# Performance work log

Measured on AMD Instinct MI355X. Metric: run time of the kernel, lower is better.

The kernel has to match this reference:

```python
import jax, jax.numpy as jnp
import numpy as np

B, S, C = 2, 2048, 1024
U, H = 1024, 16
FFH = int(U * 4.0)
NEG = -1e9
EPS = 1e-5


def setup_inputs() -> dict:
    key = jax.random.key(0)
    ks = jax.random.split(key, 16)
    w = lambda k, sh: jax.random.normal(k, sh, dtype=jnp.float32) * 0.02
    return {
        'x': jax.random.normal(ks[0], (B, S, C), dtype=jnp.float32),
        'wq': w(ks[1], (C, U)), 'bq': jnp.zeros((U,), jnp.float32),
        'wk': w(ks[2], (C, U)), 'bk': jnp.zeros((U,), jnp.float32),
        'wv': w(ks[3], (C, U)), 'bv': jnp.zeros((U,), jnp.float32),
        'wf1': w(ks[4], (U, FFH)), 'bf1': jnp.zeros((FFH,), jnp.float32),
        'wf2': w(ks[5], (FFH, U)), 'bf2': jnp.zeros((U,), jnp.float32),
        'ln_g': jnp.ones((S, U), jnp.float32), 'ln_b': jnp.zeros((S, U), jnp.float32),
        'ffln_g': jnp.ones((S, U), jnp.float32), 'ffln_b': jnp.zeros((S, U), jnp.float32),
    }


def _ln2d(x, g, b):
    # LayerNorm over last two dims ([len_ts, units]) as in nn.LayerNorm([S, U])
    m = jnp.mean(x, axis=(-2, -1), keepdims=True)
    v = jnp.mean(jnp.square(x - m), axis=(-2, -1), keepdims=True)
    return (x - m) * jax.lax.rsqrt(v + EPS) * g + b


def reference(x, wq, bq, wk, bk, wv, bv, wf1, bf1, wf2, bf2, ln_g, ln_b, ffln_g, ffln_b):
    dh = U // H
    Q = (x @ wq + bq).reshape(B, S, H, dh)
    K = (x @ wk + bk).reshape(B, S, H, dh)
    V = (x @ wv + bv).reshape(B, S, H, dh)
    scores = jnp.einsum('bqhd,bkhd->bhqk', Q, K) / jnp.sqrt(jnp.float32(dh))
    mask = jnp.tril(jnp.ones((S, S), dtype=bool))  # causal tril buffer
    scores = jnp.where(mask, scores, NEG)
    attn = jax.nn.softmax(scores, axis=-1)
    out = jnp.einsum('bhqk,bkhd->bqhd', attn, V).reshape(B, S, U)
    out = out + x  # residual
    out = _ln2d(out, ln_g, ln_b)
    ff = jax.nn.relu(out @ wf1 + bf1) @ wf2 + bf2
    out = _ln2d(out + ff, ffln_g, ffln_b)
    return out
```

## Files before the change

kernel.cpp:

```cpp
#include <hip/hip_runtime.h>
#include <hip/hip_bf16.h>

typedef short s16x8 __attribute__((ext_vector_type(8)));
typedef float f32x4 __attribute__((ext_vector_type(4)));
typedef float f32x16 __attribute__((ext_vector_type(16)));
typedef unsigned short u16x4 __attribute__((ext_vector_type(4)));
typedef unsigned u32x4 __attribute__((ext_vector_type(4)));

#define DEV static __device__ __forceinline__

DEV unsigned short f2bf(float f) {
  __hip_bfloat16 h = __float2bfloat16(f);
  return *reinterpret_cast<unsigned short*>(&h);
}
DEV float bf2f(unsigned short u) {
  union { unsigned u; float f; } v; v.u = (unsigned)u << 16; return v.f;
}

#define GLDS16(src, dst) \
  __builtin_amdgcn_global_load_lds((const __attribute__((address_space(1))) void*)(src), \
                                   (__attribute__((address_space(3))) void*)(dst), 16, 0, 0)

#define MFMA(a, b, c) __builtin_amdgcn_mfma_f32_16x16x32_bf16((a), (b), (c), 0, 0, 0)
#define MFMA32(a, b, c) __builtin_amdgcn_mfma_f32_32x32x16_bf16((a), (b), (c), 0, 0, 0)

__global__ __launch_bounds__(256) void k_f32_to_bf16(const float* __restrict__ in,
                                                     unsigned short* __restrict__ out, int n4) {
  int i = blockIdx.x * 256 + threadIdx.x;
  if (i >= n4) return;
  float4 v = ((const float4*)in)[i];
  u16x4 o; o.x = f2bf(v.x); o.y = f2bf(v.y); o.z = f2bf(v.z); o.w = f2bf(v.w);
  ((u16x4*)out)[i] = o;
}

__global__ __launch_bounds__(256) void k_transpose_w(const float* __restrict__ W,
                                                     unsigned short* __restrict__ Wt,
                                                     int K, int N, float scale) {
  __shared__ float t[64][65];
  int k0 = blockIdx.x * 64, n0 = blockIdx.y * 64;
  int tid = threadIdx.x;
#pragma unroll
  for (int i = 0; i < 16; ++i) {
    int idx = tid + i * 256; int r = idx >> 6, c = idx & 63;
    t[r][c] = W[(size_t)(k0 + r) * N + (n0 + c)];
  }
  __syncthreads();
#pragma unroll
  for (int i = 0; i < 16; ++i) {
    int idx = tid + i * 256; int r = idx >> 6, c = idx & 63;
    Wt[(size_t)(n0 + r) * K + (k0 + c)] = f2bf(t[c][r] * scale);
  }
}

__global__ void k_concat3(const float* __restrict__ a, const float* __restrict__ b,
                          const float* __restrict__ c, float* __restrict__ out, int n, float sa) {
  int i = blockIdx.x * 256 + threadIdx.x;
  if (i >= 3 * n) return;
  int j = (i < n) ? i : (i < 2 * n ? i - n : i - 2 * n);
  out[i] = (i < n) ? a[j] * sa : (i < 2 * n ? b[j] : c[j]);
}

template <int MODE>
__global__ __launch_bounds__(512, 2) void k_gemm8(
    const unsigned short* __restrict__ A, int lda,
    const unsigned short* __restrict__ Bt, int ldb,
    const float* __restrict__ bias,
    unsigned short* __restrict__ Cb, float* __restrict__ Cf, int ldc,
    int K, int nnt, size_t zstride,
    unsigned short* __restrict__ Cq, unsigned short* __restrict__ Ck,
    unsigned short* __restrict__ Cv) {
  __shared__ __align__(16) unsigned short As[2 * 2 * 8192];
  __shared__ __align__(16) unsigned short Bs[2 * 2 * 8192];
  int nwg = gridDim.x;
  int bid = blockIdx.x;
  int cpx = nwg >> 3;
  int swz = (bid & 7) * cpx + (bid >> 3);
  int mt = swz / nnt, nt = swz % nnt;
  int m0 = mt * 256, n0 = nt * 256;
  int tid = threadIdx.x, w = tid >> 6, l = tid & 63;
  int wm = (w >> 2) * 128, wn = (w & 3) * 64;
  int kb = blockIdx.z * K;

  int sr = tid >> 2;
  int gsrc = (tid & 3) ^ ((sr >> 1) & 3);
  const unsigned short* Ag0 = A + (size_t)(m0 + sr) * lda + kb + gsrc * 8;
  const unsigned short* Ag1 = Ag0 + (size_t)128 * lda;
  const unsigned short* Bg0 = Bt + (size_t)(n0 + sr) * ldb + kb + gsrc * 8;
  const unsigned short* Bg1 = Bg0 + (size_t)128 * ldb;

#define STG_A(t, kh) do { int _c = (t) * 64 + (kh) * 32; int _d = ((((t) & 1) * 2 + (kh)) * 8192); \
    GLDS16(Ag0 + _c, &As[_d + tid * 8]); GLDS16(Ag1 + _c, &As[_d + 4096 + tid * 8]); } while (0)
#define STG_B(t, kh) do { int _c = (t) * 64 + (kh) * 32; int _d = ((((t) & 1) * 2 + (kh)) * 8192); \
    GLDS16(Bg0 + _c, &Bs[_d + tid * 8]); GLDS16(Bg1 + _c, &Bs[_d + 4096 + tid * 8]); } while (0)

  int lswz = (l >> 1) & 3;
  int acol = ((l >> 4) ^ lswz) * 8;
  const unsigned short* Afr = &As[(wm + (l & 15)) * 32 + acol];
  const unsigned short* Bfr = &Bs[(wn + (l & 15)) * 32 + acol];

  f32x4 acc[8][4] = {};
  int nkt = K >> 6;

  STG_A(0, 0); STG_B(0, 0); STG_A(0, 1); STG_B(0, 1); STG_A(1, 0); STG_B(1, 0);
  asm volatile("s_waitcnt vmcnt(4)" ::: "memory");
  __builtin_amdgcn_s_barrier();
  __builtin_amdgcn_sched_barrier(0);

  for (int t = 0; t < nkt; ++t) {
    int cur = t & 1, rem = nkt - t;
    const unsigned short* ab = Afr + cur * 16384;
    const unsigned short* bb = Bfr + cur * 16384;
    s16x8 af[4], bf[4];
    if (t + 1 < nkt) STG_A(t + 1, 1);
#pragma unroll
    for (int nr = 0; nr < 4; ++nr) bf[nr] = *(const s16x8*)(bb + nr * 512);
#pragma unroll
    for (int mr = 0; mr < 4; ++mr) af[mr] = *(const s16x8*)(ab + mr * 512);
    __builtin_amdgcn_s_setprio(1);
#pragma unroll
    for (int mr = 0; mr < 4; ++mr)
#pragma unroll
      for (int nr = 0; nr < 4; ++nr)
        acc[mr][nr] = MFMA(af[mr], bf[nr], acc[mr][nr]);
    __builtin_amdgcn_s_setprio(0);
    if (t + 1 < nkt) STG_B(t + 1, 1);
#pragma unroll
    for (int mr = 0; mr < 4; ++mr) af[mr] = *(const s16x8*)(ab + 2048 + mr * 512);
    __builtin_amdgcn_s_setprio(1);
#pragma unroll
    for (int mr = 0; mr < 4; ++mr)
#pragma unroll
      for (int nr = 0; nr < 4; ++nr)
        acc[mr + 4][nr] = MFMA(af[mr], bf[nr], acc[mr + 4][nr]);
    __builtin_amdgcn_s_setprio(0);
    if (rem >= 2) { asm volatile("s_waitcnt vmcnt(4)" ::: "memory"); }
    else          { asm volatile("s_waitcnt vmcnt(0)" ::: "memory"); }
    __builtin_amdgcn_s_barrier();
    __builtin_amdgcn_sched_barrier(0);
    if (t + 2 < nkt) STG_A(t + 2, 0);
#pragma unroll
    for (int nr = 0; nr < 4; ++nr) bf[nr] = *(const s16x8*)(bb + 8192 + nr * 512);
#pragma unroll
    for (int mr = 0; mr < 4; ++mr) af[mr] = *(const s16x8*)(ab + 8192 + mr * 512);
    __builtin_amdgcn_s_setprio(1);
#pragma unroll
    for (int mr = 0; mr < 4; ++mr)
#pragma unroll
      for (int nr = 0; nr < 4; ++nr)
        acc[mr][nr] = MFMA(af[mr], bf[nr], acc[mr][nr]);
    __builtin_amdgcn_s_setprio(0);
    if (t + 2 < nkt) STG_B(t + 2, 0);
#pragma unroll
    for (int mr = 0; mr < 4; ++mr) af[mr] = *(const s16x8*)(ab + 8192 + 2048 + mr * 512);
    __builtin_amdgcn_s_setprio(1);
#pragma unroll
    for (int mr = 0; mr < 4; ++mr)
#pragma unroll
      for (int nr = 0; nr < 4; ++nr)
        acc[mr + 4][nr] = MFMA(af[mr], bf[nr], acc[mr + 4][nr]);
    __builtin_amdgcn_s_setprio(0);
    if (rem >= 3) { asm volatile("s_waitcnt vmcnt(4)" ::: "memory"); }
    else          { asm volatile("s_waitcnt vmcnt(0)" ::: "memory"); }
    __builtin_amdgcn_s_barrier();
    __builtin_amdgcn_sched_barrier(0);
  }
#undef STG_A
#undef STG_B

  if (MODE == 4) {
    if (nt < 8) {
      unsigned short* dst = (nt < 4) ? Cq : Ck;
      int cb = (nt < 4) ? 0 : 1024;
#pragma unroll
      for (int mr = 0; mr < 8; ++mr) {
        int rb = m0 + wm + mr * 16 + (l >> 4) * 4;
#pragma unroll
        for (int nr = 0; nr < 4; ++nr) {
          int col = n0 + wn + nr * 16 + (l & 15);
          float bv = bias[col];
#pragma unroll
          for (int j = 0; j < 4; ++j)
            dst[(size_t)(rb + j) * 1024 + (col - cb)] = f2bf(acc[mr][nr][j] + bv);
        }
      }
    } else {
#pragma unroll
      for (int mr = 0; mr < 8; ++mr) {
        int rb = m0 + wm + mr * 16 + (l >> 4) * 4;
        int b2 = rb >> 11, s2 = rb & 2047;
        int s2p = (s2 & ~12) | ((s2 & 4) << 1) | ((s2 & 8) >> 1);
#pragma unroll
        for (int nr = 0; nr < 4; ++nr) {
          int col2 = n0 - 2048 + wn + nr * 16 + (l & 15);
          float bv = bias[col2 + 2048];
          u16x4 pk;
#pragma unroll
          for (int j = 0; j < 4; ++j) ((unsigned short*)&pk)[j] = f2bf(acc[mr][nr][j] + bv);
          *(u16x4*)(Cv + ((size_t)((b2 * 16 + (col2 >> 6)) * 64 + (col2 & 63))) * 2048 + s2p) = pk;
        }
      }
    }
    return;
  }
  unsigned short* Cbz = (MODE == 3) ? (Cb + zstride * blockIdx.z) : Cb;
#pragma unroll
  for (int mr = 0; mr < 8; ++mr) {
    int rb = m0 + wm + mr * 16 + (l >> 4) * 4;
#pragma unroll
    for (int nr = 0; nr < 4; ++nr) {
      int col = n0 + wn + nr * 16 + (l & 15);
      float bv = (MODE == 3) ? 0.f : bias[col];
#pragma unroll
      for (int j = 0; j < 4; ++j) {
        float v = acc[mr][nr][j] + bv;
        size_t off = (size_t)(rb + j) * ldc + col;
        if (MODE == 1) v = fmaxf(v, 0.f);
        Cbz[off] = f2bf(v);
      }
    }
  }
}

__global__ __launch_bounds__(256) void k_ff2_reduce(
    unsigned short* __restrict__ slices, const float* __restrict__ bias,
    const unsigned short* __restrict__ resid, float* __restrict__ partials) {
  __shared__ float red[8];
  int i = blockIdx.x;
  size_t rb = (size_t)i * 4096;
  int c = threadIdx.x * 4;
  u16x4 a0 = *(const u16x4*)(slices + rb + c);
  u16x4 a1 = *(const u16x4*)(slices + rb + 1024 + c);
  u16x4 a2 = *(const u16x4*)(slices + rb + 2048 + c);
  u16x4 a3 = *(const u16x4*)(slices + rb + 3072 + c);
  float4 bv = *(const float4*)(bias + c);
  u16x4 rv = *(const u16x4*)(resid + (size_t)i * 1024 + c);
  float4 o;
  o.x = bf2f(a0.x) + bf2f(a1.x) + bf2f(a2.x) + bf2f(a3.x) + bv.x + bf2f(rv.x);
  o.y = bf2f(a0.y) + bf2f(a1.y) + bf2f(a2.y) + bf2f(a3.y) + bv.y + bf2f(rv.y);
  o.z = bf2f(a0.z) + bf2f(a1.z) + bf2f(a2.z) + bf2f(a3.z) + bv.z + bf2f(rv.z);
  o.w = bf2f(a0.w) + bf2f(a1.w) + bf2f(a2.w) + bf2f(a3.w) + bv.w + bf2f(rv.w);
  __syncthreads();
  *(float4*)((float*)slices + (size_t)i * 2048 + c) = o;
  float bsum = o.x + o.y + o.z + o.w;
  float bsq = o.x * o.x + o.y * o.y + o.z * o.z + o.w * o.w;
  int wv = threadIdx.x >> 6, lv = threadIdx.x & 63;
#pragma unroll
  for (int mk = 1; mk < 64; mk <<= 1) { bsum += __shfl_xor(bsum, mk); bsq += __shfl_xor(bsq, mk); }
  if (lv == 0) { red[wv] = bsum; red[4 + wv] = bsq; }
  __syncthreads();
  if (threadIdx.x == 0) {
    partials[i * 2] = red[0] + red[1] + red[2] + red[3];
    partials[i * 2 + 1] = red[4] + red[5] + red[6] + red[7];
  }
}

__global__ __launch_bounds__(128, 2) void k_attn(
    const unsigned short* __restrict__ Qg, const unsigned short* __restrict__ Kg,
    const unsigned short* __restrict__ Vt,
    const float* __restrict__ x, unsigned short* __restrict__ hpre,
    float* __restrict__ partials, int S, int H) {
  __shared__ __align__(16) unsigned short Ks[2][4096];
  __shared__ __align__(16) unsigned short Vs[2][4096];
  __shared__ float ascr[2][32];
  __shared__ float red[4];
  int bh = blockIdx.x, b = bh >> 4, h = bh & 15;
  const int nqt = S / 64;
  int qt = nqt - 1 - (int)blockIdx.y;
  int tid = threadIdx.x, w = tid >> 6, l = tid & 63;
  int lo = l & 31, hi5 = l >> 5;
  const int U = H * 64;
  const unsigned short* Qb = Qg + (size_t)(b * S) * 1024 + h * 64;
  const unsigned short* Kb = Kg + (size_t)(b * S) * 1024 + h * 64;
  const unsigned short* Vb = Vt + (size_t)bh * 64 * S;

  int sr8 = l >> 3;
  int sc8 = ((l & 7) ^ (sr8 & 7)) * 8;
  unsigned short* KsW = &Ks[w][0];
  unsigned short* VsW = &Vs[w][0];
#define STG_K(kt) do { int _kn = (kt) * 64; \
    _Pragma("unroll") for (int i2 = 0; i2 < 8; ++i2) \
      GLDS16(Kb + (size_t)(_kn + i2 * 8 + sr8) * 1024 + sc8, KsW + i2 * 512 + l * 8); } while (0)
#define STG_V(kt) do { int _kn = (kt) * 64; \
    _Pragma("unroll") for (int i2 = 0; i2 < 8; ++i2) \
      GLDS16(Vb + (size_t)(i2 * 8 + sr8) * S + _kn + sc8, VsW + i2 * 512 + l * 8); } while (0)

  int qrow = qt * 64 + w * 32 + lo;
  s16x8 qf[4];
#pragma unroll
  for (int s = 0; s < 4; ++s)
    qf[s] = *(const s16x8*)(Qb + (size_t)qrow * 1024 + s * 16 + hi5 * 8);

  int krow[16];
#pragma unroll
  for (int r = 0; r < 16; ++r) krow[r] = (r & 3) + 8 * (r >> 2) + 4 * hi5;

  f32x16 o0 = {}, o1 = {};
  float m = -1e30f, lsum = 0.f;

  STG_K(0); STG_V(0);

  for (int kt = 0; kt <= qt; ++kt) {
    asm volatile("s_waitcnt vmcnt(8)" ::: "memory");
    __builtin_amdgcn_sched_barrier(0);
    f32x16 sc0 = {}, sc1 = {};
    __builtin_amdgcn_s_setprio(1);
#pragma unroll
    for (int s = 0; s < 4; ++s) {
      int gc = ((2 * s + hi5) ^ (lo & 7)) * 8;
      s16x8 kf0 = *(const s16x8*)&KsW[lo * 64 + gc];
      s16x8 kf1 = *(const s16x8*)&KsW[(32 + lo) * 64 + gc];
      sc0 = MFMA32(kf0, qf[s], sc0);
      sc1 = MFMA32(kf1, qf[s], sc1);
    }
    __builtin_amdgcn_s_setprio(0);
    asm volatile("s_waitcnt lgkmcnt(0)" ::: "memory");
    __builtin_amdgcn_sched_barrier(0);
    if (kt < qt) STG_K(kt + 1);
    if (kt == qt) {
      int wq = w * 32 + lo;
#pragma unroll
      for (int r = 0; r < 16; ++r) {
        if (krow[r] > wq) sc0[r] = -1e30f;
        if (krow[r] + 32 > wq) sc1[r] = -1e30f;
      }
    }
    float mx = sc0[0];
#pragma unroll
    for (int r = 1; r < 16; ++r) mx = fmaxf(mx, sc0[r]);
#pragma unroll
    for (int r = 0; r < 16; ++r) mx = fmaxf(mx, sc1[r]);
    mx = fmaxf(mx, __shfl_xor(mx, 32));
    if (__ballot(mx > m + 11.5415603f)) {
      float mnew = fmaxf(m, mx);
      float alpha = __builtin_amdgcn_exp2f(m - mnew);
      m = mnew;
      lsum *= alpha;
      if (l < 32) ascr[w][lo] = alpha;
#pragma unroll
      for (int r = 0; r < 16; ++r) {
        float aj = ascr[w][krow[r]];
        o0[r] *= aj; o1[r] *= aj;
      }
    }
    float rs = 0.f;
    unsigned wk0[8], wk1[8];
#pragma unroll
    for (int j = 0; j < 8; ++j) {
      float p0 = __builtin_amdgcn_exp2f(sc0[2 * j] - m);
      float p1 = __builtin_amdgcn_exp2f(sc0[2 * j + 1] - m);
      rs += p0 + p1;
      wk0[j] = (unsigned)f2bf(p0) | ((unsigned)f2bf(p1) << 16);
      float p2 = __builtin_amdgcn_exp2f(sc1[2 * j] - m);
      float p3 = __builtin_amdgcn_exp2f(sc1[2 * j + 1] - m);
      rs += p2 + p3;
      wk1[j] = (unsigned)f2bf(p2) | ((unsigned)f2bf(p3) << 16);
    }
    rs += __shfl_xor(rs, 32);
    lsum += rs;
    if (kt < qt) { asm volatile("s_waitcnt vmcnt(8)" ::: "memory"); }
    else         { asm volatile("s_waitcnt vmcnt(0)" ::: "memory"); }
    __builtin_amdgcn_sched_barrier(0);
    __builtin_amdgcn_s_setprio(1);
#pragma unroll
    for (int s = 0; s < 4; ++s) {
      u32x4 paw;
      if (s == 0)      { paw.x = wk0[0]; paw.y = wk0[1]; paw.z = wk0[2]; paw.w = wk0[3]; }
      else if (s == 1) { paw.x = wk0[4]; paw.y = wk0[5]; paw.z = wk0[6]; paw.w = wk0[7]; }
      else if (s == 2) { paw.x = wk1[0]; paw.y = wk1[1]; paw.z = wk1[2]; paw.w = wk1[3]; }
      else             { paw.x = wk1[4]; paw.y = wk1[5]; paw.z = wk1[6]; paw.w = wk1[7]; }
      s16x8 pa = *(s16x8*)&paw;
      int gc = ((2 * s + hi5) ^ (lo & 7)) * 8;
      s16x8 vf0 = *(const s16x8*)&VsW[lo * 64 + gc];
      s16x8 vf1 = *(const s16x8*)&VsW[(32 + lo) * 64 + gc];
      o0 = MFMA32(pa, vf0, o0);
      o1 = MFMA32(pa, vf1, o1);
    }
    __builtin_amdgcn_s_setprio(0);
    asm volatile("s_waitcnt lgkmcnt(0)" ::: "memory");
    __builtin_amdgcn_sched_barrier(0);
    if (kt < qt) STG_V(kt + 1);
  }
  if (l < 32) ascr[w][lo] = 1.f / lsum;
  float bsum = 0.f, bsq = 0.f;
  unsigned short* hb = hpre + (size_t)(b * S) * U + h * 64;
  const float* xb = x + (size_t)(b * S) * U + h * 64;
#pragma unroll
  for (int r = 0; r < 16; ++r) {
    float inv = ascr[w][krow[r]];
    int srow = qt * 64 + w * 32 + krow[r];
    size_t base = (size_t)srow * U + lo;
    float v0 = o0[r] * inv + xb[base];
    float v1 = o1[r] * inv + xb[base + 32];
    hb[base] = f2bf(v0);
    hb[base + 32] = f2bf(v1);
    bsum += v0 + v1; bsq += v0 * v0 + v1 * v1;
  }
#pragma unroll
  for (int mk = 1; mk < 64; mk <<= 1) { bsum += __shfl_xor(bsum, mk); bsq += __shfl_xor(bsq, mk); }
  if (l == 0) { red[w * 2] = bsum; red[w * 2 + 1] = bsq; }
  __syncthreads();
  if (tid == 0) {
    int pi = b * (H * nqt) + h * nqt + qt;
    partials[pi * 2] = red[0] + red[2];
    partials[pi * 2 + 1] = red[1] + red[3];
  }
#undef STG_K
#undef STG_V
}

__global__ __launch_bounds__(256) void k_ln_stats(const float* __restrict__ partials, int nper,
                                                  float* __restrict__ stats, float invN) {
  int b = blockIdx.x, tid = threadIdx.x;
  float s = 0.f, q = 0.f;
  for (int i = tid; i < nper; i += 256) { s += partials[(b * nper + i) * 2]; q += partials[(b * nper + i) * 2 + 1]; }
#pragma unroll
  for (int mk = 1; mk < 64; mk <<= 1) { s += __shfl_xor(s, mk); q += __shfl_xor(q, mk); }
  __shared__ float red[8];
  int w = tid >> 6, l = tid & 63;
  if (l == 0) { red[w] = s; red[4 + w] = q; }
  __syncthreads();
  if (tid == 0) {
    s = red[0] + red[1] + red[2] + red[3];
    q = red[4] + red[5] + red[6] + red[7];
    float m = s * invN, var = q * invN - m * m;
    stats[b * 2] = m; stats[b * 2 + 1] = rsqrtf(var + 1e-5f);
  }
}

__global__ __launch_bounds__(256) void k_ln_apply_b(
    const unsigned short* __restrict__ src, const float* __restrict__ stats,
    const float* __restrict__ g, const float* __restrict__ bt,
    unsigned short* __restrict__ outb, int SU) {
  int b = blockIdx.y;
  int idx = (blockIdx.x * 256 + threadIdx.x) * 4;
  float m = stats[b * 2], r = stats[b * 2 + 1];
  u16x4 v4 = *(const u16x4*)(src + (size_t)b * SU + idx);
  float4 gg = *(const float4*)(g + idx);
  float4 bb = *(const float4*)(bt + idx);
  u16x4 ob;
  ob.x = f2bf((bf2f(v4.x) - m) * r * gg.x + bb.x);
  ob.y = f2bf((bf2f(v4.y) - m) * r * gg.y + bb.y);
  ob.z = f2bf((bf2f(v4.z) - m) * r * gg.z + bb.z);
  ob.w = f2bf((bf2f(v4.w) - m) * r * gg.w + bb.w);
  *(u16x4*)(outb + (size_t)b * SU + idx) = ob;
}

__global__ __launch_bounds__(256) void k_ln_apply2(
    const float* __restrict__ src, const float* __restrict__ stats,
    const float* __restrict__ g, const float* __restrict__ bt,
    float* __restrict__ outf) {
  int b = blockIdx.y;
  int row = blockIdx.x;
  int grow = b * 2048 + row;
  int c = threadIdx.x * 4;
  float m = stats[b * 2], r = stats[b * 2 + 1];
  float4 v = *(const float4*)(src + (size_t)grow * 2048 + c);
  float4 gg = *(const float4*)(g + (size_t)row * 1024 + c);
  float4 bb = *(const float4*)(bt + (size_t)row * 1024 + c);
  float4 o;
  o.x = (v.x - m) * r * gg.x + bb.x;
  o.y = (v.y - m) * r * gg.y + bb.y;
  o.z = (v.z - m) * r * gg.z + bb.z;
  o.w = (v.w - m) * r * gg.w + bb.w;
  *(float4*)(outf + (size_t)grow * 1024 + c) = o;
}

extern "C" void kernel_launch(void* const* d_in, const int* in_sizes, int n_in,
                              void* d_out, int out_size, void* d_ws, size_t ws_size,
                              hipStream_t stream) {
  (void)in_sizes; (void)n_in; (void)out_size; (void)ws_size;
  const int S = 2048, H = 16;
  const float* x   = (const float*)d_in[0];
  const float* wq  = (const float*)d_in[1];
  const float* bq  = (const float*)d_in[2];
  const float* wk  = (const float*)d_in[3];
  const float* bk  = (const float*)d_in[4];
  const float* wv  = (const float*)d_in[5];
  const float* bv  = (const float*)d_in[6];
  const float* wf1 = (const float*)d_in[7];
  const float* bf1 = (const float*)d_in[8];
  const float* wf2 = (const float*)d_in[9];
  const float* bf2 = (const float*)d_in[10];
  const float* lng = (const float*)d_in[11];
  const float* lnb = (const float*)d_in[12];
  const float* ffg = (const float*)d_in[13];
  const float* ffb = (const float*)d_in[14];

  char* ws = (char*)d_ws;
  unsigned short* wqkvT = (unsigned short*)(ws);
  unsigned short* wf1T  = (unsigned short*)(ws + 6291456);
  unsigned short* wf2T  = (unsigned short*)(ws + 14680064);
  unsigned short* xb    = (unsigned short*)(ws + 23068672);
  unsigned short* qb    = (unsigned short*)(ws + 31457280);
  unsigned short* kbuf  = (unsigned short*)(ws + 39845888);
  unsigned short* vt    = (unsigned short*)(ws + 56623104);
  unsigned short* h1b   = (unsigned short*)(ws + 65011712);
  unsigned short* hpreb = (unsigned short*)(ws + 73400320);
  unsigned short* ff2s  = (unsigned short*)(ws + 73400320);
  unsigned short* f1b   = (unsigned short*)(ws + 23068672);
  float* biasqkv        = (float*)(ws + 106954752);
  float* part_attn      = (float*)(ws + 106967040);
  float* stats1         = (float*)(ws + 106977280);
  float* ffpart2        = (float*)(ws);
  float* stats2         = (float*)(ws + 65536);

  const float qscale = 0.125f * 1.44269504f;
  k_f32_to_bf16<<<4096, 256, 0, stream>>>(x, xb, 4096 * 1024 / 4);
  k_transpose_w<<<dim3(16, 16), 256, 0, stream>>>(wq, wqkvT, 1024, 1024, qscale);
  k_transpose_w<<<dim3(16, 16), 256, 0, stream>>>(wk, wqkvT + 1024 * 1024, 1024, 1024, 1.0f);
  k_transpose_w<<<dim3(16, 16), 256, 0, stream>>>(wv, wqkvT + 2048 * 1024, 1024, 1024, 1.0f);
  k_transpose_w<<<dim3(16, 64), 256, 0, stream>>>(wf1, wf1T, 1024, 4096, 1.0f);
  k_transpose_w<<<dim3(64, 16), 256, 0, stream>>>(wf2, wf2T, 4096, 1024, 1.0f);
  k_concat3<<<12, 256, 0, stream>>>(bq, bk, bv, biasqkv, 1024, qscale);

  k_gemm8<4><<<dim3(192, 1, 1), 512, 0, stream>>>(xb, 1024, wqkvT, 1024, biasqkv,
      nullptr, nullptr, 0, 1024, 12, 0, qb, kbuf, vt);

  k_attn<<<dim3(32, 32), 128, 0, stream>>>(qb, kbuf, vt, x, hpreb, part_attn, S, H);

  k_ln_stats<<<2, 256, 0, stream>>>(part_attn, 512, stats1, 1.f / (2048.f * 1024.f));
  k_ln_apply_b<<<dim3(2048, 2), 256, 0, stream>>>(hpreb, stats1, lng, lnb, h1b, S * 1024);

  k_gemm8<1><<<dim3(256, 1, 1), 512, 0, stream>>>(h1b, 1024, wf1T, 1024, bf1,
      f1b, nullptr, 4096, 1024, 16, 0, nullptr, nullptr, nullptr);

  k_gemm8<3><<<dim3(64, 1, 4), 512, 0, stream>>>(f1b, 4096, wf2T, 4096, nullptr,
      ff2s, nullptr, 4096, 1024, 4, 1024, nullptr, nullptr, nullptr);

  k_ff2_reduce<<<4096, 256, 0, stream>>>(ff2s, bf2, h1b, ffpart2);

  k_ln_stats<<<2, 256, 0, stream>>>(ffpart2, 2048, stats2, 1.f / (2048.f * 1024.f));
  k_ln_apply2<<<dim3(2048, 2), 256, 0, stream>>>((float*)ff2s, stats2, ffg, ffb, (float*)d_out);
}
```

Before: 240.5 us.

## Software-pipeline attention: overlap next-tile QK^T with current softmax/PV, share K/V loads

```diff
diff --git a/kernel.cpp b/kernel.cpp
--- a/kernel.cpp
+++ b/kernel.cpp
@@ -273,16 +273,19 @@
   const unsigned short* Kb = Kg + (size_t)(b * S) * 1024 + h * 64;
   const unsigned short* Vb = Vt + (size_t)bh * 64 * S;
 
-  int sr8 = l >> 3;
-  int sc8 = ((l & 7) ^ (sr8 & 7)) * 8;
-  unsigned short* KsW = &Ks[w][0];
-  unsigned short* VsW = &Vs[w][0];
-#define STG_K(kt) do { int _kn = (kt) * 64; \
-    _Pragma("unroll") for (int i2 = 0; i2 < 8; ++i2) \
-      GLDS16(Kb + (size_t)(_kn + i2 * 8 + sr8) * 1024 + sc8, KsW + i2 * 512 + l * 8); } while (0)
-#define STG_V(kt) do { int _kn = (kt) * 64; \
-    _Pragma("unroll") for (int i2 = 0; i2 < 8; ++i2) \
-      GLDS16(Vb + (size_t)(i2 * 8 + sr8) * S + _kn + sc8, VsW + i2 * 512 + l * 8); } while (0)
+  int sg_r[4], sg_c[4];
+#pragma unroll
+  for (int it = 0; it < 4; ++it) {
+    int g = it * 128 + tid;
+    sg_r[it] = g >> 3;
+    sg_c[it] = ((g & 7) ^ ((g >> 3) & 7)) * 8;
+  }
+#define STG_K(kt) do { int _kn = (kt) * 64, _bf = (kt) & 1; \
+    _Pragma("unroll") for (int it = 0; it < 4; ++it) \
+      GLDS16(Kb + (size_t)(_kn + sg_r[it]) * 1024 + sg_c[it], &Ks[_bf][(it * 128 + tid) * 8]); } while (0)
+#define STG_V(kt) do { int _kn = (kt) * 64, _bf = (kt) & 1; \
+    _Pragma("unroll") for (int it = 0; it < 4; ++it) \
+      GLDS16(Vb + (size_t)sg_r[it] * S + _kn + sg_c[it], &Vs[_bf][(it * 128 + tid) * 8]); } while (0)
 
   int qrow = qt * 64 + w * 32 + lo;
   s16x8 qf[4];
@@ -296,90 +299,104 @@
 
   f32x16 o0 = {}, o1 = {};
   float m = -1e30f, lsum = 0.f;
+  f32x16 scA0, scA1, scB0, scB1;
+
+#define QK_T(S0, S1, T) do { \
+    S0 = (f32x16)(0.0f); S1 = (f32x16)(0.0f); \
+    const unsigned short* _kp = &Ks[(T) & 1][0]; \
+    __builtin_amdgcn_s_setprio(1); \
+    _Pragma("unroll") for (int s = 0; s < 4; ++s) { \
+      int gc = ((2 * s + hi5) ^ (lo & 7)) * 8; \
+      s16x8 kf0 = *(const s16x8*)&_kp[lo * 64 + gc]; \
+      s16x8 kf1 = *(const s16x8*)&_kp[(32 + lo) * 64 + gc]; \
+      S0 = MFMA32(kf0, qf[s], S0); \
+      S1 = MFMA32(kf1, qf[s], S1); } \
+    __builtin_amdgcn_s_setprio(0); } while (0)
+
+#define SMPV(S0, S1, T, DOMASK) do { \
+    if (DOMASK) { int wq = w * 32 + lo; \
+      _Pragma("unroll") for (int r = 0; r < 16; ++r) { \
+        if (krow[r] > wq) S0[r] = -1e30f; \
+        if (krow[r] + 32 > wq) S1[r] = -1e30f; } } \
+    float mx = S0[0]; \
+    _Pragma("unroll") for (int r = 1; r < 16; ++r) mx = fmaxf(mx, S0[r]); \
+    _Pragma("unroll") for (int r = 0; r < 16; ++r) mx = fmaxf(mx, S1[r]); \
+    mx = fmaxf(mx, __shfl_xor(mx, 32)); \
+    if (__ballot(mx > m + 11.5415603f)) { \
+      float mnew = fmaxf(m, mx); \
+      float alpha = __builtin_amdgcn_exp2f(m - mnew); \
+      m = mnew; lsum *= alpha; \
+      if (l < 32) ascr[w][lo] = alpha; \
+      _Pragma("unroll") for (int r = 0; r < 16; ++r) { \
+        float aj = ascr[w][krow[r]]; o0[r] *= aj; o1[r] *= aj; } } \
+    float rs = 0.f; unsigned wk0[8], wk1[8]; \
+    _Pragma("unroll") for (int j = 0; j < 8; ++j) { \
+      float p0 = __builtin_amdgcn_exp2f(S0[2 * j] - m); \
+      float p1 = __builtin_amdgcn_exp2f(S0[2 * j + 1] - m); \
+      rs += p0 + p1; wk0[j] = (unsigned)f2bf(p0) | ((unsigned)f2bf(p1) << 16); \
+      float p2 = __builtin_amdgcn_exp2f(S1[2 * j] - m); \
+      float p3 = __builtin_amdgcn_exp2f(S1[2 * j + 1] - m); \
+      rs += p2 + p3; wk1[j] = (unsigned)f2bf(p2) | ((unsigned)f2bf(p3) << 16); } \
+    rs += __shfl_xor(rs, 32); lsum += rs; \
+    __builtin_amdgcn_s_setprio(1); \
+    _Pragma("unroll") for (int s = 0; s < 4; ++s) { \
+      u32x4 paw; \
+      if (s == 0)      { paw.x = wk0[0]; paw.y = wk0[1]; paw.z = wk0[2]; paw.w = wk0[3]; } \
+      else if (s == 1) { paw.x = wk0[4]; paw.y = wk0[5]; paw.z = wk0[6]; paw.w = wk0[7]; } \
+      else if (s == 2) { paw.x = wk1[0]; paw.y = wk1[1]; paw.z = wk1[2]; paw.w = wk1[3]; } \
+      else             { paw.x = wk1[4]; paw.y = wk1[5]; paw.z = wk1[6]; paw.w = wk1[7]; } \
+      s16x8 pa = *(s16x8*)&paw; \
+      int gc = ((2 * s + hi5) ^ (lo & 7)) * 8; \
+      s16x8 vf0 = *(const s16x8*)&Vs[(T) & 1][lo * 64 + gc]; \
+      s16x8 vf1 = *(const s16x8*)&Vs[(T) & 1][(32 + lo) * 64 + gc]; \
+      o0 = MFMA32(pa, vf0, o0); \
+      o1 = MFMA32(pa, vf1, o1); } \
+    __builtin_amdgcn_s_setprio(0); \
+  } while (0)
+
+#define BODY(O0, O1, I0, I1, T) do { \
+    asm volatile("s_waitcnt vmcnt(4)" ::: "memory"); \
+    __builtin_amdgcn_s_barrier(); \
+    __builtin_amdgcn_sched_barrier(0); \
+    if ((T) + 1 <= qt) STG_K((T) + 1); \
+    QK_T(O0, O1, (T)); \
+    SMPV(I0, I1, (T) - 1, false); \
+    asm volatile("s_waitcnt lgkmcnt(0)" ::: "memory"); \
+    __builtin_amdgcn_sched_barrier(0); \
+    __builtin_amdgcn_s_barrier(); \
+    __builtin_amdgcn_sched_barrier(0); \
+    if ((T) + 1 <= qt) STG_V((T) + 1); \
+  } while (0)
 
   STG_K(0); STG_V(0);
-
-  for (int kt = 0; kt <= qt; ++kt) {
+  if (qt >= 1) {
+    STG_K(1); STG_V(1);
     asm volatile("s_waitcnt vmcnt(8)" ::: "memory");
+  } else {
+    asm volatile("s_waitcnt vmcnt(4)" ::: "memory");
+  }
+  __builtin_amdgcn_s_barrier();
+  __builtin_amdgcn_sched_barrier(0);
+  QK_T(scA0, scA1, 0);
+  asm volatile("s_waitcnt lgkmcnt(0)" ::: "memory");
+  __builtin_amdgcn_sched_barrier(0);
+
+  int t = 1;
+  for (; t + 1 <= qt; t += 2) {
+    BODY(scB0, scB1, scA0, scA1, t);
+    BODY(scA0, scA1, scB0, scB1, t + 1);
+  }
+  if (t <= qt) {
+    BODY(scB0, scB1, scA0, scA1, t);
+    asm volatile("s_waitcnt vmcnt(0)" ::: "memory");
     __builtin_amdgcn_sched_barrier(0);
-    f32x16 sc0 = {}, sc1 = {};
-    __builtin_amdgcn_s_setprio(1);
-#pragma unroll
-    for (int s = 0; s < 4; ++s) {
-      int gc = ((2 * s + hi5) ^ (lo & 7)) * 8;
-      s16x8 kf0 = *(const s16x8*)&KsW[lo * 64 + gc];
-      s16x8 kf1 = *(const s16x8*)&KsW[(32 + lo) * 64 + gc];
-      sc0 = MFMA32(kf0, qf[s], sc0);
-      sc1 = MFMA32(kf1, qf[s], sc1);
-    }
-    __builtin_amdgcn_s_setprio(0);
-    asm volatile("s_waitcnt lgkmcnt(0)" ::: "memory");
+    SMPV(scB0, scB1, qt, true);
+  } else {
+    asm volatile("s_waitcnt vmcnt(0)" ::: "memory");
     __builtin_amdgcn_sched_barrier(0);
-    if (kt < qt) STG_K(kt + 1);
-    if (kt == qt) {
-      int wq = w * 32 + lo;
-#pragma unroll
-      for (int r = 0; r < 16; ++r) {
-        if (krow[r] > wq) sc0[r] = -1e30f;
-        if (krow[r] + 32 > wq) sc1[r] = -1e30f;
-      }
-    }
-    float mx = sc0[0];
-#pragma unroll
-    for (int r = 1; r < 16; ++r) mx = fmaxf(mx, sc0[r]);
-#pragma unroll
-    for (int r = 0; r < 16; ++r) mx = fmaxf(mx, sc1[r]);
-    mx = fmaxf(mx, __shfl_xor(mx, 32));
-    if (__ballot(mx > m + 11.5415603f)) {
-      float mnew = fmaxf(m, mx);
-      float alpha = __builtin_amdgcn_exp2f(m - mnew);
-      m = mnew;
-      lsum *= alpha;
-      if (l < 32) ascr[w][lo] = alpha;
-#pragma unroll
-      for (int r = 0; r < 16; ++r) {
-        float aj = ascr[w][krow[r]];
-        o0[r] *= aj; o1[r] *= aj;
-      }
-    }
-    float rs = 0.f;
-    unsigned wk0[8], wk1[8];
-#pragma unroll
-    for (int j = 0; j < 8; ++j) {
-      float p0 = __builtin_amdgcn_exp2f(sc0[2 * j] - m);
-      float p1 = __builtin_amdgcn_exp2f(sc0[2 * j + 1] - m);
-      rs += p0 + p1;
-      wk0[j] = (unsigned)f2bf(p0) | ((unsigned)f2bf(p1) << 16);
-      float p2 = __builtin_amdgcn_exp2f(sc1[2 * j] - m);
-      float p3 = __builtin_amdgcn_exp2f(sc1[2 * j + 1] - m);
-      rs += p2 + p3;
-      wk1[j] = (unsigned)f2bf(p2) | ((unsigned)f2bf(p3) << 16);
-    }
-    rs += __shfl_xor(rs, 32);
-    lsum += rs;
-    if (kt < qt) { asm volatile("s_waitcnt vmcnt(8)" ::: "memory"); }
-    else         { asm volatile("s_waitcnt vmcnt(0)" ::: "memory"); }
-    __builtin_amdgcn_sched_barrier(0);
-    __builtin_amdgcn_s_setprio(1);
-#pragma unroll
-    for (int s = 0; s < 4; ++s) {
-      u32x4 paw;
-      if (s == 0)      { paw.x = wk0[0]; paw.y = wk0[1]; paw.z = wk0[2]; paw.w = wk0[3]; }
-      else if (s == 1) { paw.x = wk0[4]; paw.y = wk0[5]; paw.z = wk0[6]; paw.w = wk0[7]; }
-      else if (s == 2) { paw.x = wk1[0]; paw.y = wk1[1]; paw.z = wk1[2]; paw.w = wk1[3]; }
-      else             { paw.x = wk1[4]; paw.y = wk1[5]; paw.z = wk1[6]; paw.w = wk1[7]; }
-      s16x8 pa = *(s16x8*)&paw;
-      int gc = ((2 * s + hi5) ^ (lo & 7)) * 8;
-      s16x8 vf0 = *(const s16x8*)&VsW[lo * 64 + gc];
-      s16x8 vf1 = *(const s16x8*)&VsW[(32 + lo) * 64 + gc];
-      o0 = MFMA32(pa, vf0, o0);
-      o1 = MFMA32(pa, vf1, o1);
-    }
-    __builtin_amdgcn_s_setprio(0);
-    asm volatile("s_waitcnt lgkmcnt(0)" ::: "memory");
-    __builtin_amdgcn_sched_barrier(0);
-    if (kt < qt) STG_V(kt + 1);
-  }
+    SMPV(scA0, scA1, qt, true);
+  }
+
   if (l < 32) ascr[w][lo] = 1.f / lsum;
   float bsum = 0.f, bsq = 0.f;
   unsigned short* hb = hpre + (size_t)(b * S) * U + h * 64;
@@ -406,6 +423,9 @@
   }
 #undef STG_K
 #undef STG_V
+#undef QK_T
+#undef SMPV
+#undef BODY
 }
 
 __global__ __launch_bounds__(256) void k_ln_stats(const float* __restrict__ partials, int nper,
```

Result: faster. 233.4 us (-3.0%).
